# Kernel tuning notes

Hardware: AMD Instinct MI355X
Metric: run time of the kernel (lower is better)

## Reference

```python
import jax, jax.numpy as jnp
import numpy as np

DELTA_V = 0.5
DELTA_D = 3.0
NUM_LABELS = 5  # labels 0..4 -> C = max label = 4


def setup_inputs() -> dict:
    key = jax.random.key(0)
    k1, k2 = jax.random.split(key)
    B, E, H, W = 16, 8, 512, 1024
    pred = jax.random.normal(k1, (B, E, H, W), dtype=jnp.float32)
    instance_label = jax.random.randint(k2, (B, H, W), 0, NUM_LABELS).astype(jnp.int32)
    binary_label = (instance_label > 0).astype(jnp.float32)[:, None]  # [B,1,H,W]
    return {"pred": pred, "binary_label": binary_label, "instance_label": instance_label}


def reference(pred, binary_label, instance_label):
    # pred: [B,E,H,W], binary_label: [B,1,H,W], instance_label: [B,H,W] int
    B, E, H, W = pred.shape
    L = NUM_LABELS
    C = L - 1  # int(instance_label.max()) with labels 0..L-1
    dtype = pred.dtype

    pred_roi = binary_label * pred                                  # [B,E,H,W]
    masks = jax.nn.one_hot(instance_label, L, dtype=dtype)          # [B,H,W,L]

    counts = jnp.einsum('bhwl->bl', masks)                          # [B,L] pixels per cluster
    sums = jnp.einsum('behw,bhwl->ble', pred_roi, masks)            # [B,L,E]
    sumsq = jnp.einsum('behw,bhwl->bl', pred_roi * pred_roi, masks)  # [B,L]

    mu = sums / counts[..., None]                                   # [B,L,E] cluster means

    # torch.norm(mu - xi) is the Frobenius norm over the whole [E,Nc] cluster:
    # ||mu - xi||_F^2 = sum(mask*x^2) - Nc*||mu||^2
    frob_sq = sumsq - counts * jnp.sum(mu * mu, axis=-1)            # [B,L]
    pos = frob_sq > 0
    n = jnp.where(pos, jnp.sqrt(jnp.where(pos, frob_sq, 1.0)), 0.0)  # safe sqrt
    var = jnp.where(n > DELTA_V, (n - DELTA_V) ** 2, 0.0)           # [B,L]
    L_var = jnp.sum(var, axis=1) / C                                # [B]

    # dist term: pairs (i,j), i != j, over means of labels 0..C-1 (original loop bound)
    mu_d = mu[:, :C]                                                # [B,C,E]
    diff = mu_d[:, :, None, :] - mu_d[:, None, :, :]                # [B,C,C,E]
    dsq = jnp.sum(diff * diff, axis=-1)                             # [B,C,C]
    offdiag = (1.0 - jnp.eye(C, dtype=dtype))[None]                 # [1,C,C]
    ok = (dsq > 0) & (offdiag > 0)
    d = jnp.sqrt(jnp.where(ok, dsq, 1.0))
    hinge = jnp.where(ok, jax.nn.relu(DELTA_D - d) ** 2,
                      jnp.where(offdiag > 0, DELTA_D ** 2, 0.0))
    L_dist = jnp.sum(hinge, axis=(1, 2))                            # [B]

    return jnp.mean(L_var) + jnp.mean(L_dist)
```

## Files before the change

### kernel.cpp

```cpp
#include <hip/hip_runtime.h>

#define NB 16
#define NE 8
#define NH 512
#define NW 1024
#define HW (NH * NW)
#define CHUNKS 64
#define TPB 256
#define PIX_PER_CHUNK (HW / CHUNKS)
#define GROUPS (PIX_PER_CHUNK / (TPB * 4))
#define ACC_STRIDE 40

__global__ __launch_bounds__(TPB) void cluster_partial(
    const float* __restrict__ pred, const int* __restrict__ lab,
    float* __restrict__ acc)
{
    const int b     = blockIdx.x / CHUNKS;
    const int chunk = blockIdx.x % CHUNKS;
    const int t     = threadIdx.x;

    const float* predb = pred + (long)b * NE * HW;
    const int*   labb  = lab  + (long)b * HW;
    const int chunkbase = chunk * PIX_PER_CHUNK;

    float sums[4][NE];
    float ssq_acc[4] = {0.f, 0.f, 0.f, 0.f};
    float cnt[4]     = {0.f, 0.f, 0.f, 0.f};
#pragma unroll
    for (int l = 0; l < 4; ++l)
#pragma unroll
        for (int e = 0; e < NE; ++e) sums[l][e] = 0.f;

    for (int g = 0; g < GROUPS; ++g) {
        const int pixoff = chunkbase + ((g * TPB + t) << 2);

        const int4 l4 = *reinterpret_cast<const int4*>(labb + pixoff);
        const int labs[4] = {l4.x, l4.y, l4.z, l4.w};

        float m[4][4];
#pragma unroll
        for (int p = 0; p < 4; ++p)
#pragma unroll
            for (int l = 0; l < 4; ++l)
                m[p][l] = (labs[p] == l + 1) ? 1.0f : 0.0f;

        float ssq[4] = {0.f, 0.f, 0.f, 0.f};
#pragma unroll
        for (int e = 0; e < NE; ++e) {
            const float4 v =
                *reinterpret_cast<const float4*>(predb + (long)e * HW + pixoff);
            const float vv[4] = {v.x, v.y, v.z, v.w};
#pragma unroll
            for (int p = 0; p < 4; ++p) {
                ssq[p] = fmaf(vv[p], vv[p], ssq[p]);
#pragma unroll
                for (int l = 0; l < 4; ++l)
                    sums[l][e] = fmaf(m[p][l], vv[p], sums[l][e]);
            }
        }
#pragma unroll
        for (int p = 0; p < 4; ++p)
#pragma unroll
            for (int l = 0; l < 4; ++l) {
                ssq_acc[l] = fmaf(m[p][l], ssq[p], ssq_acc[l]);
                cnt[l] += m[p][l];
            }
    }

    float vals[ACC_STRIDE];
#pragma unroll
    for (int l = 0; l < 4; ++l) {
        vals[l]     = cnt[l];
        vals[4 + l] = ssq_acc[l];
#pragma unroll
        for (int e = 0; e < NE; ++e) vals[8 + l * NE + e] = sums[l][e];
    }
#pragma unroll
    for (int i = 0; i < ACC_STRIDE; ++i) {
        float v = vals[i];
        v += __shfl_down(v, 32);
        v += __shfl_down(v, 16);
        v += __shfl_down(v, 8);
        v += __shfl_down(v, 4);
        v += __shfl_down(v, 2);
        v += __shfl_down(v, 1);
        vals[i] = v;
    }

    __shared__ float red[TPB / 64][ACC_STRIDE];
    const int wave = t >> 6;
    const int lane = t & 63;
    if (lane == 0) {
#pragma unroll
        for (int i = 0; i < ACC_STRIDE; ++i) red[wave][i] = vals[i];
    }
    __syncthreads();
    if (t < ACC_STRIDE) {
        float s = red[0][t] + red[1][t] + red[2][t] + red[3][t];
        atomicAdd(&acc[b * ACC_STRIDE + t], s);
    }
}

__global__ __launch_bounds__(64) void cluster_finalize(
    const float* __restrict__ acc, float* __restrict__ out)
{
    const int t = threadIdx.x;
    float Lb = 0.f;
    if (t < NB) {
        const float* a = acc + t * ACC_STRIDE;
        float mu[4][NE];
#pragma unroll
        for (int e = 0; e < NE; ++e) mu[0][e] = 0.f;

        float Lvar = 0.f;
#pragma unroll
        for (int l = 1; l <= 4; ++l) {
            const float c   = a[l - 1];
            const float ssq = a[4 + (l - 1)];
            float mloc[NE];
            float musq = 0.f;
#pragma unroll
            for (int e = 0; e < NE; ++e) {
                mloc[e] = a[8 + (l - 1) * NE + e] / c;
                musq = fmaf(mloc[e], mloc[e], musq);
            }
            const float frob = ssq - c * musq;
            const float n = (frob > 0.f) ? sqrtf(frob) : 0.f;
            const float dv = n - 0.5f;
            Lvar += (n > 0.5f) ? dv * dv : 0.f;
            if (l < 4) {
#pragma unroll
                for (int e = 0; e < NE; ++e) mu[l][e] = mloc[e];
            }
        }
        Lvar *= 0.25f;

        float Ldist = 0.f;
#pragma unroll
        for (int i = 0; i < 4; ++i)
#pragma unroll
            for (int j = i + 1; j < 4; ++j) {
                float dsq = 0.f;
#pragma unroll
                for (int e = 0; e < NE; ++e) {
                    const float d = mu[i][e] - mu[j][e];
                    dsq = fmaf(d, d, dsq);
                }
                float h;
                if (dsq > 0.f) {
                    const float d = sqrtf(dsq);
                    float r = 3.0f - d;
                    r = (r > 0.f) ? r : 0.f;
                    h = r * r;
                } else {
                    h = 9.0f;
                }
                Ldist += 2.0f * h;
            }

        Lb = (Lvar + Ldist) * (1.0f / NB);
    }
    Lb += __shfl_down(Lb, 32);
    Lb += __shfl_down(Lb, 16);
    Lb += __shfl_down(Lb, 8);
    Lb += __shfl_down(Lb, 4);
    Lb += __shfl_down(Lb, 2);
    Lb += __shfl_down(Lb, 1);
    if (t == 0) out[0] = Lb;
}

extern "C" void kernel_launch(void* const* d_in, const int* in_sizes, int n_in,
                              void* d_out, int out_size, void* d_ws, size_t ws_size,
                              hipStream_t stream) {
    const float* pred = (const float*)d_in[0];
    const int* lab = (const int*)d_in[2];
    float* out = (float*)d_out;
    float* acc = (float*)d_ws;

    hipMemsetAsync(acc, 0, NB * ACC_STRIDE * sizeof(float), stream);
    cluster_partial<<<NB * CHUNKS, TPB, 0, stream>>>(pred, lab, acc);
    cluster_finalize<<<1, 64, 0, stream>>>(acc, out);
}
```

Baseline: 397.4 us.

## Use more chunks, nontemporal loads, and per-block slots instead of atomics

Raises the chunk count so the grid has four times as many blocks, and fully unrolls the per-thread group loop. Pred and label loads become nontemporal vector loads. Each block now writes its partial sums to its own slot instead of issuing atomicAdds into a zeroed accumulator, which also removes the memset launch. The finalize kernel grows to 256 threads, reduces the slots per batch with wave shuffles, then computes the loss; in exchange it reads more slot data serially.

```diff
diff --git a/kernel.cpp b/kernel.cpp
--- a/kernel.cpp
+++ b/kernel.cpp
@@ -5,23 +5,28 @@
 #define NH 512
 #define NW 1024
 #define HW (NH * NW)
-#define CHUNKS 64
+#define CHUNKS 256
+#define NBLK (NB * CHUNKS)
 #define TPB 256
 #define PIX_PER_CHUNK (HW / CHUNKS)
 #define GROUPS (PIX_PER_CHUNK / (TPB * 4))
 #define ACC_STRIDE 40
 
+typedef float v4f __attribute__((ext_vector_type(4)));
+typedef int   v4i __attribute__((ext_vector_type(4)));
+
 __global__ __launch_bounds__(TPB) void cluster_partial(
     const float* __restrict__ pred, const int* __restrict__ lab,
-    float* __restrict__ acc)
+    float* __restrict__ slots)
 {
-    const int b     = blockIdx.x / CHUNKS;
-    const int chunk = blockIdx.x % CHUNKS;
+    const int bid   = blockIdx.x;
+    const int b     = bid / CHUNKS;
+    const int chunk = bid % CHUNKS;
     const int t     = threadIdx.x;
 
     const float* predb = pred + (long)b * NE * HW;
     const int*   labb  = lab  + (long)b * HW;
-    const int chunkbase = chunk * PIX_PER_CHUNK;
+    const int base0 = chunk * PIX_PER_CHUNK + (t << 2);
 
     float sums[4][NE];
     float ssq_acc[4] = {0.f, 0.f, 0.f, 0.f};
@@ -31,10 +36,12 @@
 #pragma unroll
         for (int e = 0; e < NE; ++e) sums[l][e] = 0.f;
 
+#pragma unroll
     for (int g = 0; g < GROUPS; ++g) {
-        const int pixoff = chunkbase + ((g * TPB + t) << 2);
-
-        const int4 l4 = *reinterpret_cast<const int4*>(labb + pixoff);
+        const int off = base0 + g * (TPB * 4);
+
+        const v4i l4 = __builtin_nontemporal_load(
+            reinterpret_cast<const v4i*>(labb + off));
         const int labs[4] = {l4.x, l4.y, l4.z, l4.w};
 
         float m[4][4];
@@ -47,8 +54,8 @@
         float ssq[4] = {0.f, 0.f, 0.f, 0.f};
 #pragma unroll
         for (int e = 0; e < NE; ++e) {
-            const float4 v =
-                *reinterpret_cast<const float4*>(predb + (long)e * HW + pixoff);
+            const v4f v = __builtin_nontemporal_load(
+                reinterpret_cast<const v4f*>(predb + (long)e * HW + off));
             const float vv[4] = {v.x, v.y, v.z, v.w};
 #pragma unroll
             for (int p = 0; p < 4; ++p) {
@@ -77,14 +84,14 @@
     }
 #pragma unroll
     for (int i = 0; i < ACC_STRIDE; ++i) {
-        float v = vals[i];
-        v += __shfl_down(v, 32);
-        v += __shfl_down(v, 16);
-        v += __shfl_down(v, 8);
-        v += __shfl_down(v, 4);
-        v += __shfl_down(v, 2);
-        v += __shfl_down(v, 1);
-        vals[i] = v;
+        float vv = vals[i];
+        vv += __shfl_down(vv, 32);
+        vv += __shfl_down(vv, 16);
+        vv += __shfl_down(vv, 8);
+        vv += __shfl_down(vv, 4);
+        vv += __shfl_down(vv, 2);
+        vv += __shfl_down(vv, 1);
+        vals[i] = vv;
     }
 
     __shared__ float red[TPB / 64][ACC_STRIDE];
@@ -96,77 +103,102 @@
     }
     __syncthreads();
     if (t < ACC_STRIDE) {
-        float s = red[0][t] + red[1][t] + red[2][t] + red[3][t];
-        atomicAdd(&acc[b * ACC_STRIDE + t], s);
+        const float s = red[0][t] + red[1][t] + red[2][t] + red[3][t];
+        slots[t * NBLK + bid] = s;
     }
 }
 
-__global__ __launch_bounds__(64) void cluster_finalize(
-    const float* __restrict__ acc, float* __restrict__ out)
+__global__ __launch_bounds__(256) void cluster_finalize(
+    const float* __restrict__ slots, float* __restrict__ out)
 {
-    const int t = threadIdx.x;
-    float Lb = 0.f;
-    if (t < NB) {
-        const float* a = acc + t * ACC_STRIDE;
-        float mu[4][NE];
-#pragma unroll
-        for (int e = 0; e < NE; ++e) mu[0][e] = 0.f;
-
-        float Lvar = 0.f;
-#pragma unroll
-        for (int l = 1; l <= 4; ++l) {
-            const float c   = a[l - 1];
-            const float ssq = a[4 + (l - 1)];
-            float mloc[NE];
-            float musq = 0.f;
-#pragma unroll
-            for (int e = 0; e < NE; ++e) {
-                mloc[e] = a[8 + (l - 1) * NE + e] / c;
-                musq = fmaf(mloc[e], mloc[e], musq);
+    const int t    = threadIdx.x;
+    const int wave = t >> 6;
+    const int lane = t & 63;
+    __shared__ float wsum[4];
+
+    float wacc = 0.f;
+    for (int bi = 0; bi < 4; ++bi) {
+        const int b = wave * 4 + bi;
+        float vals[ACC_STRIDE];
+#pragma unroll
+        for (int i = 0; i < ACC_STRIDE; ++i) {
+            float s = 0.f;
+#pragma unroll
+            for (int k = 0; k < 4; ++k)
+                s += slots[i * NBLK + b * CHUNKS + lane + 64 * k];
+            vals[i] = s;
+        }
+#pragma unroll
+        for (int i = 0; i < ACC_STRIDE; ++i) {
+            float v = vals[i];
+            v += __shfl_down(v, 32);
+            v += __shfl_down(v, 16);
+            v += __shfl_down(v, 8);
+            v += __shfl_down(v, 4);
+            v += __shfl_down(v, 2);
+            v += __shfl_down(v, 1);
+            vals[i] = v;
+        }
+
+        if (lane == 0) {
+            float mu[4][NE];
+#pragma unroll
+            for (int e = 0; e < NE; ++e) mu[0][e] = 0.f;
+
+            float Lvar = 0.f;
+#pragma unroll
+            for (int l = 1; l <= 4; ++l) {
+                const float c   = vals[l - 1];
+                const float ssq = vals[4 + (l - 1)];
+                float mloc[NE];
+                float musq = 0.f;
+#pragma unroll
+                for (int e = 0; e < NE; ++e) {
+                    mloc[e] = vals[8 + (l - 1) * NE + e] / c;
+                    musq = fmaf(mloc[e], mloc[e], musq);
+                }
+                const float frob = ssq - c * musq;
+                const float n = (frob > 0.f) ? sqrtf(frob) : 0.f;
+                const float dv = n - 0.5f;
+                Lvar += (n > 0.5f) ? dv * dv : 0.f;
+                if (l < 4) {
+#pragma unroll
+                    for (int e = 0; e < NE; ++e) mu[l][e] = mloc[e];
+                }
             }
-            const float frob = ssq - c * musq;
-            const float n = (frob > 0.f) ? sqrtf(frob) : 0.f;
-            const float dv = n - 0.5f;
-            Lvar += (n > 0.5f) ? dv * dv : 0.f;
-            if (l < 4) {
-#pragma unroll
-                for (int e = 0; e < NE; ++e) mu[l][e] = mloc[e];
-            }
-        }
-        Lvar *= 0.25f;
-
-        float Ldist = 0.f;
-#pragma unroll
-        for (int i = 0; i < 4; ++i)
-#pragma unroll
-            for (int j = i + 1; j < 4; ++j) {
-                float dsq = 0.f;
-#pragma unroll
-                for (int e = 0; e < NE; ++e) {
-                    const float d = mu[i][e] - mu[j][e];
-                    dsq = fmaf(d, d, dsq);
+            Lvar *= 0.25f;
+
+            float Ldist = 0.f;
+#pragma unroll
+            for (int i = 0; i < 4; ++i)
+#pragma unroll
+                for (int j = i + 1; j < 4; ++j) {
+                    float dsq = 0.f;
+#pragma unroll
+                    for (int e = 0; e < NE; ++e) {
+                        const float d = mu[i][e] - mu[j][e];
+                        dsq = fmaf(d, d, dsq);
+                    }
+                    float h;
+                    if (dsq > 0.f) {
+                        const float d = sqrtf(dsq);
+                        float r = 3.0f - d;
+                        r = (r > 0.f) ? r : 0.f;
+                        h = r * r;
+                    } else {
+                        h = 9.0f;
+                    }
+                    Ldist += 2.0f * h;
                 }
-                float h;
-                if (dsq > 0.f) {
-                    const float d = sqrtf(dsq);
-                    float r = 3.0f - d;
-                    r = (r > 0.f) ? r : 0.f;
-                    h = r * r;
-                } else {
-                    h = 9.0f;
-                }
-                Ldist += 2.0f * h;
-            }
-
-        Lb = (Lvar + Ldist) * (1.0f / NB);
-    }
-    Lb += __shfl_down(Lb, 32);
-    Lb += __shfl_down(Lb, 16);
-    Lb += __shfl_down(Lb, 8);
-    Lb += __shfl_down(Lb, 4);
-    Lb += __shfl_down(Lb, 2);
-    Lb += __shfl_down(Lb, 1);
-    if (t == 0) out[0] = Lb;
+
+            wacc += Lvar + Ldist;
+        }
+    }
+
+    if (lane == 0) wsum[wave] = wacc;
+    __syncthreads();
+    if (t == 0)
+        out[0] = (wsum[0] + wsum[1] + wsum[2] + wsum[3]) * (1.0f / NB);
 }
 
 extern "C" void kernel_launch(void* const* d_in, const int* in_sizes, int n_in,
@@ -175,9 +207,8 @@
     const float* pred = (const float*)d_in[0];
     const int* lab = (const int*)d_in[2];
     float* out = (float*)d_out;
-    float* acc = (float*)d_ws;
-
-    hipMemsetAsync(acc, 0, NB * ACC_STRIDE * sizeof(float), stream);
-    cluster_partial<<<NB * CHUNKS, TPB, 0, stream>>>(pred, lab, acc);
-    cluster_finalize<<<1, 64, 0, stream>>>(acc, out);
+    float* slots = (float*)d_ws;
+
+    cluster_partial<<<NBLK, TPB, 0, stream>>>(pred, lab, slots);
+    cluster_finalize<<<1, 256, 0, stream>>>(slots, out);
 }
```

Result: no change. 397.6 us (+0.0%).
